# Performance work log

Measured on AMD Instinct MI355X. Metric: run time of the kernel, lower is better.

The kernel has to match this reference:

```python
import jax, jax.numpy as jnp
import numpy as np

MAX_SHIFT = 64  # init kwarg; alpha=None -> score_max branch


def setup_inputs() -> dict:
    key = jax.random.key(0)
    k1, k2 = jax.random.split(key)
    x = jax.random.normal(k1, (64, 2, 4096), dtype=jnp.float32)
    y = jax.random.normal(k2, (64, 2, 4096), dtype=jnp.float32)
    return {"x": x, "y": y}


def reference(x, y):
    S = MAX_SHIFT
    W = 2 * S + 1  # num_windows
    # forward(): flip along channel axis
    x = jnp.flip(x, axis=1)
    B, C, D = x.shape
    # min-max normalize each (batch, channel) trace to [-1, 1]
    xmin = x.min(axis=-1, keepdims=True)
    xmax = x.max(axis=-1, keepdims=True)
    x = 2 * (x - xmin) / (xmax - xmin) - 1
    # torch.hann_window(dim) is periodic: 0.5*(1 - cos(2*pi*n/N))
    hann = 0.5 * (1.0 - jnp.cos(2.0 * jnp.pi * jnp.arange(D, dtype=x.dtype) / D))
    x = x * hann
    # pad by max_shift on both sides, then take W sliding windows of length D
    xpad = jnp.pad(x, ((0, 0), (0, 0), (S, S)))  # [B, C, D+2S]
    idx = jnp.arange(W)[:, None] + jnp.arange(D)[None, :]  # [W, D]
    xw = xpad[:, :, idx]  # [B, C, W, D] (matches torch unfold+reshape)
    xw = jnp.transpose(xw, (2, 0, 1, 3))  # [W, B, C, D]
    # mean-centered Pearson correlation per window
    xc = xw - xw.mean(axis=-1, keepdims=True)
    yc = y - y.mean(axis=-1, keepdims=True)
    corr = jnp.sum(xc * yc, axis=-1)  # [W, B, C]
    norm = jnp.sum(xc * xc, axis=-1) * jnp.sum(yc * yc, axis=-1)
    corr = corr / jnp.sqrt(norm)
    # alpha is None -> score_max: max over shifts, L2 over channels
    values = corr.max(axis=0)  # [B, C]
    scores = jnp.sqrt(jnp.sum(values ** 2, axis=-1))  # [B]
    return -scores.mean()
```

## Files before the change

### kernel.cpp

```cpp
#include <hip/hip_runtime.h>
#include <math.h>

#define DD      4096
#define SSHIFT  64
#define WW      129
#define PADN    (DD + 2 * SSHIFT)
#define NPART   4
#define BLOCKN  256

__global__ __launch_bounds__(BLOCKN) void spl_main(
        const float* __restrict__ x, const float* __restrict__ y,
        float* __restrict__ partial) {
    const int blk  = blockIdx.x;
    const int bc   = blk >> 2;
    const int part = blk & (NPART - 1);
    const int b = bc >> 1;
    const int c = bc & 1;
    const float* xp = x + (size_t)(b * 2 + (1 - c)) * DD;
    const float* yp = y + (size_t)(b * 2 + c) * DD;

    __shared__ __align__(16) float xs[PADN];
    __shared__ float P0s[65], P0q[65], Qs[65], Qq[65];
    __shared__ float red[20];
    __shared__ float wred[4];

    const int tid  = threadIdx.x;
    const int lane = tid & 63;
    const int wv   = tid >> 6;

    const float4* xp4 = (const float4*)xp;
    const float4* yp4 = (const float4*)yp;
    float xmn = 3.0e38f, xmx = -3.0e38f, ysum = 0.0f;
    #pragma unroll
    for (int it = 0; it < DD / 4 / BLOCKN; ++it) {
        int d4 = tid + it * BLOCKN;
        float4 xv = xp4[d4];
        xmn = fminf(xmn, fminf(fminf(xv.x, xv.y), fminf(xv.z, xv.w)));
        xmx = fmaxf(xmx, fmaxf(fmaxf(xv.x, xv.y), fmaxf(xv.z, xv.w)));
        float4 yv = yp4[d4];
        ysum += (yv.x + yv.y) + (yv.z + yv.w);
    }
    #pragma unroll
    for (int off = 32; off > 0; off >>= 1) {
        xmn  = fminf(xmn, __shfl_down(xmn, off, 64));
        xmx  = fmaxf(xmx, __shfl_down(xmx, off, 64));
        ysum += __shfl_down(ysum, off, 64);
    }
    if (lane == 0) { red[wv] = xmn; red[4 + wv] = xmx; red[8 + wv] = ysum; }
    __syncthreads();
    xmn = fminf(fminf(red[0], red[1]), fminf(red[2], red[3]));
    xmx = fmaxf(fmaxf(red[4], red[5]), fmaxf(red[6], red[7]));
    const float ymean = (red[8] + red[9] + red[10] + red[11]) * (1.0f / (float)DD);
    const float inv   = 2.0f / (xmx - xmn);

    float ssum = 0.0f, ssq = 0.0f;
    for (int m = tid; m < PADN; m += BLOCKN) {
        int d = m + part - SSHIFT;
        float v = 0.0f;
        if (d >= 0 && d < DD) {
            float h = 0.5f * (1.0f - __builtin_amdgcn_cosf((float)d * (1.0f / (float)DD)));
            v = (inv * (xp[d] - xmn) - 1.0f) * h;
        }
        xs[m] = v;
        ssum += v;
        ssq  = fmaf(v, v, ssq);
    }
    #pragma unroll
    for (int off = 32; off > 0; off >>= 1) {
        ssum += __shfl_down(ssum, off, 64);
        ssq  += __shfl_down(ssq,  off, 64);
    }
    if (lane == 0) { red[12 + wv] = ssum; red[16 + wv] = ssq; }

    float4 yc4[16];
    float syy = 0.0f;
    #pragma unroll
    for (int i = 0; i < 16; ++i) {
        float4 v = yp4[64 * i + lane];
        v.x -= ymean; v.y -= ymean; v.z -= ymean; v.w -= ymean;
        yc4[i] = v;
        syy = fmaf(v.x, v.x, fmaf(v.y, v.y, fmaf(v.z, v.z, fmaf(v.w, v.w, syy))));
    }
    #pragma unroll
    for (int off = 32; off > 0; off >>= 1) syy += __shfl_down(syy, off, 64);
    syy = __shfl(syy, 0, 64);

    __syncthreads();
    const float Stot  = (red[12] + red[13]) + (red[14] + red[15]);
    const float Sqtot = (red[16] + red[17]) + (red[18] + red[19]);

    if (wv == 0) {
        float v = xs[SSHIFT - part + lane];
        float s = v, sq = v * v, vsq = sq;
        #pragma unroll
        for (int off = 1; off < 64; off <<= 1) {
            float t  = __shfl_up(s,  off, 64);
            float tq = __shfl_up(sq, off, 64);
            if (lane >= off) { s += t; sq += tq; }
        }
        P0s[lane + 1] = s; P0q[lane + 1] = sq;
        if (lane == 0) { P0s[0] = 0.0f; P0q[0] = 0.0f; }
        (void)vsq;
    } else if (wv == 1) {
        float v = xs[DD - part + lane];
        float s = v, sq = v * v;
        #pragma unroll
        for (int off = 1; off < 64; off <<= 1) {
            float t  = __shfl_up(s,  off, 64);
            float tq = __shfl_up(sq, off, 64);
            if (lane >= off) { s += t; sq += tq; }
        }
        float Ts = __shfl(s, 63, 64), Tq = __shfl(sq, 63, 64);
        Qs[lane] = Ts - (s - v);
        Qq[lane] = Tq - (sq - v * v);
        if (lane == 63) { Qs[64] = 0.0f; Qq[64] = 0.0f; }
    }
    __syncthreads();

    const float4* xs4 = (const float4*)xs;
    const int w0 = part + 4 * wv;
    float vmax = -3.0e38f;
    #pragma unroll
    for (int k = 0; k < 9; ++k) {
        const int w = w0 + 16 * k;
        if (w < WW) {
            const int q = wv + 4 * k;
            float cr = 0.0f;
            #pragma unroll
            for (int i = 0; i < 16; ++i) {
                float4 xv = xs4[64 * i + lane + q];
                cr = fmaf(xv.x, yc4[i].x,
                     fmaf(xv.y, yc4[i].y,
                     fmaf(xv.z, yc4[i].z,
                     fmaf(xv.w, yc4[i].w, cr))));
            }
            #pragma unroll
            for (int off = 32; off > 0; off >>= 1) cr += __shfl_down(cr, off, 64);
            if (lane == 0) {
                int hidx = (w > SSHIFT) ? (w - SSHIFT) : 0;
                int tidx = (w < 64) ? w : 64;
                float sx  = Stot  - P0s[hidx] - Qs[tidx];
                float sxx = Sqtot - P0q[hidx] - Qq[tidx];
                float varx = sxx - sx * sx * (1.0f / (float)DD);
                float corr = cr / sqrtf(varx * syy);
                vmax = fmaxf(vmax, corr);
            }
        }
    }
    if (lane == 0) wred[wv] = vmax;
    __syncthreads();
    if (tid == 0)
        partial[blk] = fmaxf(fmaxf(wred[0], wred[1]), fmaxf(wred[2], wred[3]));
}

__global__ void spl_final(const float* __restrict__ partial,
                          float* __restrict__ out) {
    const int b = threadIdx.x;
    float v0 = -3.0e38f, v1 = -3.0e38f;
    #pragma unroll
    for (int p = 0; p < NPART; ++p) {
        v0 = fmaxf(v0, partial[(b * 2 + 0) * NPART + p]);
        v1 = fmaxf(v1, partial[(b * 2 + 1) * NPART + p]);
    }
    float s = sqrtf(v0 * v0 + v1 * v1);
    #pragma unroll
    for (int off = 32; off > 0; off >>= 1) s += __shfl_down(s, off, 64);
    if (b == 0) out[0] = -s * (1.0f / 64.0f);
}

extern "C" void kernel_launch(void* const* d_in, const int* in_sizes, int n_in,
                              void* d_out, int out_size, void* d_ws, size_t ws_size,
                              hipStream_t stream) {
    const float* x = (const float*)d_in[0];
    const float* y = (const float*)d_in[1];
    float* out     = (float*)d_out;
    float* partial = (float*)d_ws;

    spl_main<<<dim3(128 * NPART), dim3(BLOCKN), 0, stream>>>(x, y, partial);
    spl_final<<<dim3(1), dim3(64), 0, stream>>>(partial, out);
}
```

Baseline: 71.50 us.

## Register-block eight shifts per wave and vectorize normalized x staging

The correlation loop now computes eight consecutive window shifts per wave from three float4 shared-memory loads. The old scheme did one float4 load per shift. This raises arithmetic per LDS access and cuts the number of cross-lane reductions issued. The x normalization and windowing pass is vectorized with float4 loads and stores into an unshifted padded buffer, and only the pad regions are zeroed. The per-part shift offset is dropped, the boundary prefix sums are recomputed directly from global memory, and one barrier is removed, at the cost of higher register pressure and reloading x.

```diff
diff --git a/kernel.cpp b/kernel.cpp
--- a/kernel.cpp
+++ b/kernel.cpp
@@ -2,42 +2,41 @@
 #include <math.h>
 
 #define DD      4096
-#define SSHIFT  64
 #define WW      129
-#define PADN    (DD + 2 * SSHIFT)
-#define NPART   4
+#define XSN     4240
+#define NP      4
 #define BLOCKN  256
 
 __global__ __launch_bounds__(BLOCKN) void spl_main(
         const float* __restrict__ x, const float* __restrict__ y,
         float* __restrict__ partial) {
-    const int blk  = blockIdx.x;
-    const int bc   = blk >> 2;
-    const int part = blk & (NPART - 1);
-    const int b = bc >> 1;
-    const int c = bc & 1;
+    const int blk = blockIdx.x;
+    const int bc  = blk >> 2, p = blk & 3;
+    const int b   = bc >> 1,  c = bc & 1;
     const float* xp = x + (size_t)(b * 2 + (1 - c)) * DD;
     const float* yp = y + (size_t)(b * 2 + c) * DD;
-
-    __shared__ __align__(16) float xs[PADN];
+    const float4* xp4 = (const float4*)xp;
+    const float4* yp4 = (const float4*)yp;
+
+    __shared__ __align__(16) float xs[XSN];
     __shared__ float P0s[65], P0q[65], Qs[65], Qq[65];
     __shared__ float red[20];
     __shared__ float wred[4];
 
-    const int tid  = threadIdx.x;
-    const int lane = tid & 63;
-    const int wv   = tid >> 6;
-
-    const float4* xp4 = (const float4*)xp;
-    const float4* yp4 = (const float4*)yp;
+    const int tid = threadIdx.x, lane = tid & 63, wv = tid >> 6;
+
+    if (tid < 36) {
+        int i4 = (tid < 16) ? tid : (1024 + tid);
+        ((float4*)xs)[i4] = make_float4(0.f, 0.f, 0.f, 0.f);
+    }
+
     float xmn = 3.0e38f, xmx = -3.0e38f, ysum = 0.0f;
     #pragma unroll
-    for (int it = 0; it < DD / 4 / BLOCKN; ++it) {
-        int d4 = tid + it * BLOCKN;
-        float4 xv = xp4[d4];
+    for (int it = 0; it < 4; ++it) {
+        float4 xv = xp4[tid + 256 * it];
+        float4 yv = yp4[tid + 256 * it];
         xmn = fminf(xmn, fminf(fminf(xv.x, xv.y), fminf(xv.z, xv.w)));
         xmx = fmaxf(xmx, fmaxf(fmaxf(xv.x, xv.y), fmaxf(xv.z, xv.w)));
-        float4 yv = yp4[d4];
         ysum += (yv.x + yv.y) + (yv.z + yv.w);
     }
     #pragma unroll
@@ -51,26 +50,29 @@
     xmn = fminf(fminf(red[0], red[1]), fminf(red[2], red[3]));
     xmx = fmaxf(fmaxf(red[4], red[5]), fmaxf(red[6], red[7]));
     const float ymean = (red[8] + red[9] + red[10] + red[11]) * (1.0f / (float)DD);
-    const float inv   = 2.0f / (xmx - xmn);
+    const float a   = 2.0f / (xmx - xmn);
+    const float bsh = -a * xmn - 1.0f;
 
     float ssum = 0.0f, ssq = 0.0f;
-    for (int m = tid; m < PADN; m += BLOCKN) {
-        int d = m + part - SSHIFT;
-        float v = 0.0f;
-        if (d >= 0 && d < DD) {
-            float h = 0.5f * (1.0f - __builtin_amdgcn_cosf((float)d * (1.0f / (float)DD)));
-            v = (inv * (xp[d] - xmn) - 1.0f) * h;
-        }
-        xs[m] = v;
-        ssum += v;
-        ssq  = fmaf(v, v, ssq);
-    }
-    #pragma unroll
-    for (int off = 32; off > 0; off >>= 1) {
-        ssum += __shfl_down(ssum, off, 64);
-        ssq  += __shfl_down(ssq,  off, 64);
-    }
-    if (lane == 0) { red[12 + wv] = ssum; red[16 + wv] = ssq; }
+    #pragma unroll
+    for (int it = 0; it < 4; ++it) {
+        int i4 = tid + 256 * it;
+        float4 xv = xp4[i4];
+        float fd = (float)(4 * i4);
+        float4 h;
+        h.x = 0.5f - 0.5f * __builtin_amdgcn_cosf((fd + 0.0f) * (1.0f / (float)DD));
+        h.y = 0.5f - 0.5f * __builtin_amdgcn_cosf((fd + 1.0f) * (1.0f / (float)DD));
+        h.z = 0.5f - 0.5f * __builtin_amdgcn_cosf((fd + 2.0f) * (1.0f / (float)DD));
+        h.w = 0.5f - 0.5f * __builtin_amdgcn_cosf((fd + 3.0f) * (1.0f / (float)DD));
+        float4 v;
+        v.x = fmaf(a, xv.x, bsh) * h.x;
+        v.y = fmaf(a, xv.y, bsh) * h.y;
+        v.z = fmaf(a, xv.z, bsh) * h.z;
+        v.w = fmaf(a, xv.w, bsh) * h.w;
+        ((float4*)(xs + 64))[i4] = v;
+        ssum += (v.x + v.y) + (v.z + v.w);
+        ssq = fmaf(v.x, v.x, fmaf(v.y, v.y, fmaf(v.z, v.z, fmaf(v.w, v.w, ssq))));
+    }
 
     float4 yc4[16];
     float syy = 0.0f;
@@ -82,16 +84,19 @@
         syy = fmaf(v.x, v.x, fmaf(v.y, v.y, fmaf(v.z, v.z, fmaf(v.w, v.w, syy))));
     }
     #pragma unroll
-    for (int off = 32; off > 0; off >>= 1) syy += __shfl_down(syy, off, 64);
+    for (int off = 32; off > 0; off >>= 1) {
+        ssum += __shfl_down(ssum, off, 64);
+        ssq  += __shfl_down(ssq,  off, 64);
+        syy  += __shfl_down(syy,  off, 64);
+    }
+    if (lane == 0) { red[12 + wv] = ssum; red[16 + wv] = ssq; }
     syy = __shfl(syy, 0, 64);
 
-    __syncthreads();
-    const float Stot  = (red[12] + red[13]) + (red[14] + red[15]);
-    const float Sqtot = (red[16] + red[17]) + (red[18] + red[19]);
-
     if (wv == 0) {
-        float v = xs[SSHIFT - part + lane];
-        float s = v, sq = v * v, vsq = sq;
+        int d = lane;
+        float h = 0.5f - 0.5f * __builtin_amdgcn_cosf((float)d * (1.0f / (float)DD));
+        float v = fmaf(a, xp[d], bsh) * h;
+        float s = v, sq = v * v;
         #pragma unroll
         for (int off = 1; off < 64; off <<= 1) {
             float t  = __shfl_up(s,  off, 64);
@@ -100,9 +105,10 @@
         }
         P0s[lane + 1] = s; P0q[lane + 1] = sq;
         if (lane == 0) { P0s[0] = 0.0f; P0q[0] = 0.0f; }
-        (void)vsq;
     } else if (wv == 1) {
-        float v = xs[DD - part + lane];
+        int d = 4032 + lane;
+        float h = 0.5f - 0.5f * __builtin_amdgcn_cosf((float)d * (1.0f / (float)DD));
+        float v = fmaf(a, xp[d], bsh) * h;
         float s = v, sq = v * v;
         #pragma unroll
         for (int off = 1; off < 64; off <<= 1) {
@@ -116,34 +122,49 @@
         if (lane == 63) { Qs[64] = 0.0f; Qq[64] = 0.0f; }
     }
     __syncthreads();
+    const float Stot  = (red[12] + red[13]) + (red[14] + red[15]);
+    const float Sqtot = (red[16] + red[17]) + (red[18] + red[19]);
 
     const float4* xs4 = (const float4*)xs;
-    const int w0 = part + 4 * wv;
     float vmax = -3.0e38f;
-    #pragma unroll
-    for (int k = 0; k < 9; ++k) {
-        const int w = w0 + 16 * k;
-        if (w < WW) {
-            const int q = wv + 4 * k;
-            float cr = 0.0f;
+    for (int g = p + 4 * wv; g <= 16; g += 16) {
+        float cr[8];
+        #pragma unroll
+        for (int j = 0; j < 8; ++j) cr[j] = 0.0f;
+        const int A0 = lane + 2 * g;
+        #pragma unroll
+        for (int i = 0; i < 16; ++i) {
+            int A = 64 * i + A0;
+            float4 x0 = xs4[A], x1 = xs4[A + 1], x2 = xs4[A + 2];
+            float wnd[12] = { x0.x, x0.y, x0.z, x0.w,
+                              x1.x, x1.y, x1.z, x1.w,
+                              x2.x, x2.y, x2.z, x2.w };
+            float4 yv = yc4[i];
             #pragma unroll
-            for (int i = 0; i < 16; ++i) {
-                float4 xv = xs4[64 * i + lane + q];
-                cr = fmaf(xv.x, yc4[i].x,
-                     fmaf(xv.y, yc4[i].y,
-                     fmaf(xv.z, yc4[i].z,
-                     fmaf(xv.w, yc4[i].w, cr))));
-            }
+            for (int j = 0; j < 8; ++j)
+                cr[j] = fmaf(yv.x, wnd[j],
+                        fmaf(yv.y, wnd[j + 1],
+                        fmaf(yv.z, wnd[j + 2],
+                        fmaf(yv.w, wnd[j + 3], cr[j]))));
+        }
+        #pragma unroll
+        for (int off = 32; off > 0; off >>= 1) {
             #pragma unroll
-            for (int off = 32; off > 0; off >>= 1) cr += __shfl_down(cr, off, 64);
-            if (lane == 0) {
-                int hidx = (w > SSHIFT) ? (w - SSHIFT) : 0;
-                int tidx = (w < 64) ? w : 64;
-                float sx  = Stot  - P0s[hidx] - Qs[tidx];
-                float sxx = Sqtot - P0q[hidx] - Qq[tidx];
-                float varx = sxx - sx * sx * (1.0f / (float)DD);
-                float corr = cr / sqrtf(varx * syy);
-                vmax = fmaxf(vmax, corr);
+            for (int j = 0; j < 8; ++j) cr[j] += __shfl_down(cr[j], off, 64);
+        }
+        if (lane == 0) {
+            #pragma unroll
+            for (int j = 0; j < 8; ++j) {
+                int w = 8 * g + j;
+                if (w < WW) {
+                    int hidx = (w > 64) ? (w - 64) : 0;
+                    int tidx = (w < 64) ? w : 64;
+                    float sx   = Stot  - P0s[hidx] - Qs[tidx];
+                    float sxx  = Sqtot - P0q[hidx] - Qq[tidx];
+                    float varx = sxx - sx * sx * (1.0f / (float)DD);
+                    float corr = cr[j] / sqrtf(varx * syy);
+                    vmax = fmaxf(vmax, corr);
+                }
             }
         }
     }
@@ -158,9 +179,9 @@
     const int b = threadIdx.x;
     float v0 = -3.0e38f, v1 = -3.0e38f;
     #pragma unroll
-    for (int p = 0; p < NPART; ++p) {
-        v0 = fmaxf(v0, partial[(b * 2 + 0) * NPART + p]);
-        v1 = fmaxf(v1, partial[(b * 2 + 1) * NPART + p]);
+    for (int pp = 0; pp < NP; ++pp) {
+        v0 = fmaxf(v0, partial[(b * 2 + 0) * NP + pp]);
+        v1 = fmaxf(v1, partial[(b * 2 + 1) * NP + pp]);
     }
     float s = sqrtf(v0 * v0 + v1 * v1);
     #pragma unroll
@@ -176,6 +197,6 @@
     float* out     = (float*)d_out;
     float* partial = (float*)d_ws;
 
-    spl_main<<<dim3(128 * NPART), dim3(BLOCKN), 0, stream>>>(x, y, partial);
+    spl_main<<<dim3(128 * NP), dim3(BLOCKN), 0, stream>>>(x, y, partial);
     spl_final<<<dim3(1), dim3(64), 0, stream>>>(partial, out);
 }
```

Measured after the change: 69.75 us. -2.4%, faster.
